# Optimization experiments

Measured on AMD Instinct MI355X. Metric: run time of the kernel, lower is better.

The kernel has to match this reference:

```python
import jax, jax.numpy as jnp
import numpy as np

N_NODES = 50000   # total nodes across batched graphs
N_EDGES = 100000  # molecular-like sparsity, avg degree ~2
N_GRAPHS = 2048
NUM_FEAT = 14
DIM = 64

def _gru_cell(x, h, w_ih, w_hh, b_ih, b_hh):
    # torch GRU gate order: reset, update, new
    gi = x @ w_ih.T + b_ih
    gh = h @ w_hh.T + b_hh
    ir, iz, in_ = jnp.split(gi, 3, axis=-1)
    hr, hz, hn = jnp.split(gh, 3, axis=-1)
    r = jax.nn.sigmoid(ir + hr)
    z = jax.nn.sigmoid(iz + hz)
    n = jnp.tanh(in_ + r * hn)
    return (1.0 - z) * n + z * h

def _lstm_cell(x, h, c, w_ih, w_hh, b_ih, b_hh):
    # torch LSTM gate order: input, forget, cell, output
    g = x @ w_ih.T + b_ih + h @ w_hh.T + b_hh
    i, f, gg, o = jnp.split(g, 4, axis=-1)
    c2 = jax.nn.sigmoid(f) * c + jax.nn.sigmoid(i) * jnp.tanh(gg)
    h2 = jax.nn.sigmoid(o) * jnp.tanh(c2)
    return h2, c2

def _forward(x, edge_attr, lin0_w, lin0_b, nn_w1, nn_b1, nn_w2, nn_b2,
             conv_root, conv_bias, gru_w_ih, gru_w_hh, gru_b_ih, gru_b_hh,
             s2s_w_ih, s2s_w_hh, s2s_b_ih, s2s_b_hh, lin1_w, lin1_b,
             lin2_w, lin2_b, edge_index, batch):
    N, D = x.shape[0], DIM
    src, dst = edge_index[0], edge_index[1]
    out = jax.nn.relu(x @ lin0_w.T + lin0_b)  # [N, D]
    h = out
    # edge-conditioned weight matrices: [E, D, D]
    ew = (jax.nn.relu(edge_attr @ nn_w1.T + nn_b1) @ nn_w2.T + nn_b2).reshape(-1, D, D)
    deg = jax.ops.segment_sum(jnp.ones_like(src, jnp.float32), dst, num_segments=N)
    inv_deg = 1.0 / jnp.maximum(deg, 1.0)
    for _ in range(3):
        msg = jnp.einsum('ei,eio->eo', out[src], ew)  # per-edge matvec
        agg = jax.ops.segment_sum(msg, dst, num_segments=N) * inv_deg[:, None]
        m = jax.nn.relu(out @ conv_root + agg + conv_bias)
        h = _gru_cell(m, h, gru_w_ih, gru_w_hh, gru_b_ih, gru_b_hh)
        out = h
    # Set2Set pooling, processing_steps=3
    B = N_GRAPHS
    q_star = jnp.zeros((B, 2 * D), x.dtype)
    hh = jnp.zeros((B, D), x.dtype)
    cc = jnp.zeros((B, D), x.dtype)
    for _ in range(3):
        hh, cc = _lstm_cell(q_star, hh, cc, s2s_w_ih, s2s_w_hh, s2s_b_ih, s2s_b_hh)
        e = jnp.sum(out * hh[batch], axis=-1)  # [N]
        e = e - jax.ops.segment_max(e, batch, num_segments=B)[batch]
        a = jnp.exp(e)
        a = a / (jax.ops.segment_sum(a, batch, num_segments=B)[batch] + 1e-16)
        r = jax.ops.segment_sum(a[:, None] * out, batch, num_segments=B)
        q_star = jnp.concatenate([hh, r], axis=-1)  # [B, 2D]
    y = jax.nn.relu(q_star @ lin1_w.T + lin1_b)
    y = y @ lin2_w.T + lin2_b
    return y.reshape(-1)

def setup_inputs():
    key = jax.random.key(0)
    ks = jax.random.split(key, 16)
    def rn(k, shape, scale=0.1):
        return jax.random.normal(k, shape, jnp.float32) * scale
    D = DIM
    return {
        'x': jax.random.normal(ks[0], (N_NODES, NUM_FEAT), jnp.float32),
        'edge_index': jax.random.randint(ks[1], (2, N_EDGES), 0, N_NODES),
        'edge_attr': jax.random.normal(ks[2], (N_EDGES, 4), jnp.float32),
        'batch': jnp.sort(jax.random.randint(ks[3], (N_NODES,), 0, N_GRAPHS)),
        'lin0_w': rn(ks[4], (D, NUM_FEAT)), 'lin0_b': jnp.zeros((D,), jnp.float32),
        'nn_w1': rn(ks[5], (128, 4)), 'nn_b1': jnp.zeros((128,), jnp.float32),
        'nn_w2': rn(ks[6], (D * D, 128), 0.02), 'nn_b2': jnp.zeros((D * D,), jnp.float32),
        'conv_root': rn(ks[7], (D, D)), 'conv_bias': jnp.zeros((D,), jnp.float32),
        'gru_w_ih': rn(ks[8], (3 * D, D)), 'gru_w_hh': rn(ks[9], (3 * D, D)),
        'gru_b_ih': jnp.zeros((3 * D,), jnp.float32), 'gru_b_hh': jnp.zeros((3 * D,), jnp.float32),
        's2s_w_ih': rn(ks[10], (4 * D, 2 * D)), 's2s_w_hh': rn(ks[11], (4 * D, D)),
        's2s_b_ih': jnp.zeros((4 * D,), jnp.float32), 's2s_b_hh': jnp.zeros((4 * D,), jnp.float32),
        'lin1_w': rn(ks[12], (D, 2 * D)), 'lin1_b': jnp.zeros((D,), jnp.float32),
        'lin2_w': rn(ks[13], (1, D)), 'lin2_b': jnp.zeros((1,), jnp.float32),
    }

def reference(x, edge_index, edge_attr, batch, lin0_w, lin0_b, nn_w1, nn_b1,
              nn_w2, nn_b2, conv_root, conv_bias, gru_w_ih, gru_w_hh, gru_b_ih,
              gru_b_hh, s2s_w_ih, s2s_w_hh, s2s_b_ih, s2s_b_hh, lin1_w, lin1_b,
              lin2_w, lin2_b):
    return _forward(x, edge_attr, lin0_w, lin0_b, nn_w1, nn_b1, nn_w2, nn_b2,
                    conv_root, conv_bias, gru_w_ih, gru_w_hh, gru_b_ih, gru_b_hh,
                    s2s_w_ih, s2s_w_hh, s2s_b_ih, s2s_b_hh, lin1_w, lin1_b,
                    lin2_w, lin2_b, edge_index, batch)
```

## Files before the change

### kernel.cpp

```cpp
#include <hip/hip_runtime.h>
#include <hip/hip_bf16.h>

#define NN 50000
#define NE 100000
#define NG 2048
#define NF 14
#define D 64
#define EB 128

typedef __attribute__((ext_vector_type(8))) short bf16x8;
typedef __attribute__((ext_vector_type(4))) float f32x4;

__device__ __forceinline__ float sigmoidf(float x) { return 1.f / (1.f + expf(-x)); }

__global__ void cvt_bf16_kernel(const float* __restrict__ src, __hip_bfloat16* __restrict__ dst, int n) {
    int i = blockIdx.x * 256 + threadIdx.x;
    if (i < n) dst[i] = __float2bfloat16(src[i]);
}

__global__ void transpose_kernel(const float* __restrict__ src, float* __restrict__ dst,
                                 int rows, int cols) {
    int idx = blockIdx.x * 256 + threadIdx.x;
    if (idx < rows * cols) {
        int r = idx / cols, c = idx - r * cols;
        dst[c * rows + r] = src[idx];
    }
}

__global__ void lin0_kernel(const float* __restrict__ x, const float* __restrict__ w,
                            const float* __restrict__ b, float* __restrict__ out) {
    int grp = threadIdx.x >> 6;
    int d = threadIdx.x & 63;
    int n = blockIdx.x * 4 + grp;
    __shared__ float xs[4][NF];
    int t = threadIdx.x;
    if (t < 4 * NF) {
        int r = t / NF, c = t - r * NF;
        int nn2 = blockIdx.x * 4 + r;
        xs[r][c] = (nn2 < NN) ? x[nn2 * NF + c] : 0.f;
    }
    __syncthreads();
    if (n >= NN) return;
    float acc = b[d];
#pragma unroll
    for (int k = 0; k < NF; k++) acc += xs[grp][k] * w[d * NF + k];
    out[n * D + d] = fmaxf(acc, 0.f);
}

__global__ __launch_bounds__(512, 4) void msg_mfma_kernel(
    const float* __restrict__ h, const float* __restrict__ ea,
    const float* __restrict__ w1, const float* __restrict__ b1,
    const __hip_bfloat16* __restrict__ w2r,
    const float* __restrict__ b2, const int* __restrict__ ei,
    float* __restrict__ agg)
{
    __shared__ __align__(16) char upool[34816];
    __hip_bfloat16 (*hid)[136] = (__hip_bfloat16(*)[136])upool;
    __hip_bfloat16 (*Bs)[64][136] = (__hip_bfloat16(*)[64][136])upool;
    __hip_bfloat16 (*B2s)[72] = (__hip_bfloat16(*)[72])upool;
    __shared__ __align__(16) float hsrcT[64][132];
    __shared__ float w1s[128][4];
    __shared__ float b1s[128];
    __shared__ int didx[EB];

    int tid = threadIdx.x;
    int e0 = blockIdx.x * EB;

    if (tid < 128) {
        didx[tid] = (e0 + tid < NE) ? ei[NE + e0 + tid] : -1;
    } else if (tid < 256) {
        int k = tid - 128;
        w1s[k][0] = w1[k * 4 + 0]; w1s[k][1] = w1[k * 4 + 1];
        w1s[k][2] = w1[k * 4 + 2]; w1s[k][3] = w1[k * 4 + 3];
        b1s[k] = b1[k];
    }
    {
        int e = tid >> 2, seg = (tid & 3) * 16;
        int ge = e0 + e;
        int src = (ge < NE) ? ei[ge] : 0;
        const float4* hp = (const float4*)(h + (size_t)src * 64 + seg);
#pragma unroll
        for (int u = 0; u < 4; u++) {
            float4 v = (ge < NE) ? hp[u] : make_float4(0.f, 0.f, 0.f, 0.f);
            hsrcT[seg + u * 4 + 0][e] = v.x;
            hsrcT[seg + u * 4 + 1][e] = v.y;
            hsrcT[seg + u * 4 + 2][e] = v.z;
            hsrcT[seg + u * 4 + 3][e] = v.w;
        }
    }
    __syncthreads();
    {
        int e = tid & 127, kb = (tid >> 7) * 32;
        int ge = e0 + e;
        float4 av = (ge < NE) ? *(const float4*)(ea + (size_t)ge * 4)
                              : make_float4(0.f, 0.f, 0.f, 0.f);
        for (int k = kb; k < kb + 32; k += 4) {
            union { __hip_bfloat16 b[4]; uint2 uu; } pk;
#pragma unroll
            for (int u = 0; u < 4; u++) {
                float v = b1s[k + u] + av.x * w1s[k + u][0] + av.y * w1s[k + u][1] +
                          av.z * w1s[k + u][2] + av.w * w1s[k + u][3];
                pk.b[u] = __float2bfloat16(fmaxf(v, 0.f));
            }
            *(uint2*)&hid[e][k] = pk.uu;
        }
    }
    __syncthreads();

    int lane = tid & 63;
    int wid = tid >> 6;
    int half = wid >> 2;
    int ct = wid & 3;
    int n = lane & 15, q = lane >> 4;
    int ocol = ct * 16 + n;

    bf16x8 afr[4][4];
#pragma unroll
    for (int rt = 0; rt < 4; rt++)
#pragma unroll
        for (int ks = 0; ks < 4; ks++)
            afr[rt][ks] = *(const bf16x8*)&hid[half * 64 + rt * 16 + n][ks * 32 + q * 8];
    __syncthreads();

    int srow = tid >> 3, sseg = (tid & 7) * 16;
    {
        const bf16x8* gp = (const bf16x8*)(w2r + (size_t)srow * 128 + sseg);
        bf16x8* lp = (bf16x8*)&Bs[0][srow][sseg];
        lp[0] = gp[0]; lp[1] = gp[1];
    }
    __syncthreads();

    f32x4 acc[4];
#pragma unroll
    for (int rt = 0; rt < 4; rt++) acc[rt] = (f32x4){0.f, 0.f, 0.f, 0.f};

    for (int i = 0; i < 64; i++) {
        const int cur = i & 1;
        bf16x8 pre0, pre1;
        if (i + 1 < 64) {
            const bf16x8* gp = (const bf16x8*)(w2r + (size_t)(i + 1) * 8192 + srow * 128 + sseg);
            pre0 = gp[0]; pre1 = gp[1];
        }
        bf16x8 bfr[4];
#pragma unroll
        for (int ks = 0; ks < 4; ks++)
            bfr[ks] = *(const bf16x8*)&Bs[cur][ocol][ks * 32 + q * 8];
        f32x4 S[4];
#pragma unroll
        for (int rt = 0; rt < 4; rt++) S[rt] = (f32x4){0.f, 0.f, 0.f, 0.f};
#pragma unroll
        for (int ks = 0; ks < 4; ks++)
#pragma unroll
            for (int rt = 0; rt < 4; rt++)
                S[rt] = __builtin_amdgcn_mfma_f32_16x16x32_bf16(afr[rt][ks], bfr[ks], S[rt], 0, 0, 0);
#pragma unroll
        for (int rt = 0; rt < 4; rt++) {
            f32x4 hm = *(const f32x4*)&hsrcT[i][half * 64 + rt * 16 + q * 4];
#pragma unroll
            for (int r = 0; r < 4; r++) acc[rt][r] += hm[r] * S[rt][r];
        }
        if (i + 1 < 64) {
            bf16x8* lp = (bf16x8*)&Bs[cur ^ 1][srow][sseg];
            lp[0] = pre0; lp[1] = pre1;
        }
        __syncthreads();
    }

    for (int g = tid; g < 4096; g += 512) {
        B2s[g & 63][g >> 6] = __float2bfloat16(b2[g]);
    }
    __syncthreads();
#pragma unroll
    for (int rt = 0; rt < 4; rt++) {
        f32x4 S2 = (f32x4){0.f, 0.f, 0.f, 0.f};
#pragma unroll
        for (int ks2 = 0; ks2 < 2; ks2++) {
            union { __hip_bfloat16 b[8]; bf16x8 v; } pk;
#pragma unroll
            for (int j = 0; j < 8; j++)
                pk.b[j] = __float2bfloat16(hsrcT[ks2 * 32 + q * 8 + j][half * 64 + rt * 16 + n]);
            bf16x8 bfr2 = *(const bf16x8*)&B2s[ocol][ks2 * 32 + q * 8];
            S2 = __builtin_amdgcn_mfma_f32_16x16x32_bf16(pk.v, bfr2, S2, 0, 0, 0);
        }
#pragma unroll
        for (int r = 0; r < 4; r++) acc[rt][r] += S2[r];
    }

#pragma unroll
    for (int rt = 0; rt < 4; rt++)
#pragma unroll
        for (int r = 0; r < 4; r++) {
            int e = half * 64 + rt * 16 + q * 4 + r;
            if (e0 + e < NE) {
                int dn = didx[e];
                atomicAdd(&agg[(size_t)dn * 64 + ocol], acc[rt][r]);
            }
        }
}

__global__ void deg_kernel(const int* __restrict__ ei, float* __restrict__ deg) {
    int e = blockIdx.x * 256 + threadIdx.x;
    if (e < NE) atomicAdd(&deg[ei[NE + e]], 1.0f);
}
__global__ void invdeg_kernel(float* deg) {
    int n = blockIdx.x * 256 + threadIdx.x;
    if (n < NN) deg[n] = 1.0f / fmaxf(deg[n], 1.0f);
}

__global__ __launch_bounds__(256) void conv_gru_kernel(
    float* __restrict__ h, const float* __restrict__ agg, const float* __restrict__ invdeg,
    const float* __restrict__ root, const float* __restrict__ cbias,
    const float* __restrict__ wihT, const float* __restrict__ whhT,
    const float* __restrict__ bih, const float* __restrict__ bhh)
{
    int tid = threadIdx.x;
    int grp = tid >> 6;
    int j = tid & 63;
    int n0 = blockIdx.x * 16;
    int nd0 = grp * 4;
    __shared__ float hs[16][64];
    __shared__ float ms[16][68];
    for (int i = tid; i < 1024; i += 256) {
        int nd = i >> 6, dd = i & 63;
        hs[nd][dd] = h[(n0 + nd) * D + dd];
    }
    __syncthreads();
    float mm[4] = {};
#pragma unroll 8
    for (int k = 0; k < 64; k++) {
        float rv = root[k * 64 + j];
#pragma unroll
        for (int q = 0; q < 4; q++) mm[q] += hs[nd0 + q][k] * rv;
    }
    float cb = cbias[j];
#pragma unroll
    for (int q = 0; q < 4; q++) {
        int nn2 = n0 + nd0 + q;
        float v = mm[q] + agg[(size_t)nn2 * 64 + j] * invdeg[nn2] + cb;
        ms[nd0 + q][j] = fmaxf(v, 0.f);
    }
    __syncthreads();
    float air[4] = {}, aiz[4] = {}, ain[4] = {};
    float ahr[4] = {}, ahz[4] = {}, ahn[4] = {};
#pragma unroll 4
    for (int k = 0; k < 64; k++) {
        float wr = wihT[k * 192 + j];
        float wz = wihT[k * 192 + 64 + j];
        float wn = wihT[k * 192 + 128 + j];
        float vr = whhT[k * 192 + j];
        float vz = whhT[k * 192 + 64 + j];
        float vn = whhT[k * 192 + 128 + j];
#pragma unroll
        for (int q = 0; q < 4; q++) {
            float mv = ms[nd0 + q][k], hv = hs[nd0 + q][k];
            air[q] = fmaf(mv, wr, air[q]);
            aiz[q] = fmaf(mv, wz, aiz[q]);
            ain[q] = fmaf(mv, wn, ain[q]);
            ahr[q] = fmaf(hv, vr, ahr[q]);
            ahz[q] = fmaf(hv, vz, ahz[q]);
            ahn[q] = fmaf(hv, vn, ahn[q]);
        }
    }
    float br = bih[j], bz = bih[64 + j], bn = bih[128 + j];
    float cr = bhh[j], cz = bhh[64 + j], cn = bhh[128 + j];
#pragma unroll
    for (int q = 0; q < 4; q++) {
        float r = sigmoidf(air[q] + br + ahr[q] + cr);
        float z = sigmoidf(aiz[q] + bz + ahz[q] + cz);
        float nn2 = tanhf(ain[q] + bn + r * (ahn[q] + cn));
        float hv = hs[nd0 + q][j];
        h[(n0 + nd0 + q) * D + j] = (1.f - z) * nn2 + z * hv;
    }
}

__global__ void starts_kernel(const int* __restrict__ batch, int* __restrict__ start) {
    int n = blockIdx.x * 256 + threadIdx.x;
    if (n >= NN) return;
    int b = batch[n];
    int bp = (n == 0) ? -1 : batch[n - 1];
    for (int g = bp + 1; g <= b; g++) start[g] = n;
    if (n == NN - 1) {
        for (int g = b + 1; g <= NG; g++) start[g] = NN;
    }
}

__global__ void s2s_lstm_kernel(const float* __restrict__ qstar, float* __restrict__ hh,
                                float* __restrict__ cc, const float* __restrict__ wihT,
                                const float* __restrict__ whhT, const float* __restrict__ bih,
                                const float* __restrict__ bhh) {
    int g = blockIdx.x;
    int j = threadIdx.x;
    __shared__ float q[128], hsh[64], gates[256];
    if (j < 128) q[j] = qstar[g * 128 + j];
    if (j < 64) hsh[j] = hh[g * 64 + j];
    __syncthreads();
    float acc = bih[j] + bhh[j];
#pragma unroll 8
    for (int k = 0; k < 128; k++) acc = fmaf(q[k], wihT[k * 256 + j], acc);
#pragma unroll 8
    for (int k = 0; k < 64; k++) acc = fmaf(hsh[k], whhT[k * 256 + j], acc);
    gates[j] = acc;
    __syncthreads();
    if (j < 64) {
        float gi = gates[j], gf = gates[64 + j], gg = gates[128 + j], go = gates[192 + j];
        float c2 = sigmoidf(gf) * cc[g * 64 + j] + sigmoidf(gi) * tanhf(gg);
        float h2 = sigmoidf(go) * tanhf(c2);
        cc[g * 64 + j] = c2;
        hh[g * 64 + j] = h2;
    }
}

__global__ void s2s_attn_kernel(const float* __restrict__ out, const float* __restrict__ hh,
                                const int* __restrict__ start, float* __restrict__ qstar) {
    int g = blockIdx.x;
    int tid = threadIdx.x;
    int d = tid & 63, sub = tid >> 6;
    int n0 = start[g], n1 = start[g + 1];
    float hd = hh[g * 64 + d];
    __shared__ float red[4][64];
    __shared__ float mxS[4], seS[4];
    float mx = -INFINITY;
    for (int n = n0 + sub; n < n1; n += 4) {
        float p = out[n * D + d] * hd;
#pragma unroll
        for (int off = 32; off; off >>= 1) p += __shfl_xor(p, off);
        mx = fmaxf(mx, p);
    }
    if (d == 0) mxS[sub] = mx;
    __syncthreads();
    mx = fmaxf(fmaxf(mxS[0], mxS[1]), fmaxf(mxS[2], mxS[3]));
    float sexp = 0.f, racc = 0.f;
    for (int n = n0 + sub; n < n1; n += 4) {
        float ond = out[n * D + d];
        float p = ond * hd;
#pragma unroll
        for (int off = 32; off; off >>= 1) p += __shfl_xor(p, off);
        float a = expf(p - mx);
        sexp += a;
        racc = fmaf(a, ond, racc);
    }
    red[sub][d] = racc;
    if (d == 0) seS[sub] = sexp;
    __syncthreads();
    if (sub == 0) {
        float rtot = red[0][d] + red[1][d] + red[2][d] + red[3][d];
        float stot = seS[0] + seS[1] + seS[2] + seS[3];
        float r = rtot / (stot + 1e-16f);
        qstar[g * 128 + d] = hd;
        qstar[g * 128 + 64 + d] = r;
    }
}

__global__ void final_kernel(const float* __restrict__ qstar, const float* __restrict__ w1,
                             const float* __restrict__ b1, const float* __restrict__ w2,
                             const float* __restrict__ b2, float* __restrict__ y) {
    int g = blockIdx.x;
    int d = threadIdx.x;
    __shared__ float q[128];
    q[d] = qstar[g * 128 + d];
    q[64 + d] = qstar[g * 128 + 64 + d];
    __syncthreads();
    float acc = b1[d];
#pragma unroll 8
    for (int k = 0; k < 128; k++) acc = fmaf(q[k], w1[d * 128 + k], acc);
    acc = fmaxf(acc, 0.f);
    float p = acc * w2[d];
#pragma unroll
    for (int off = 32; off; off >>= 1) p += __shfl_xor(p, off);
    if (d == 0) y[g] = p + b2[0];
}

extern "C" void kernel_launch(void* const* d_in, const int* in_sizes, int n_in,
                              void* d_out, int out_size, void* d_ws, size_t ws_size,
                              hipStream_t stream) {
    (void)in_sizes; (void)n_in; (void)out_size; (void)ws_size;
    const float* x = (const float*)d_in[0];
    const int* edge_index = (const int*)d_in[1];
    const float* edge_attr = (const float*)d_in[2];
    const int* batch = (const int*)d_in[3];
    const float* lin0_w = (const float*)d_in[4];
    const float* lin0_b = (const float*)d_in[5];
    const float* nn_w1 = (const float*)d_in[6];
    const float* nn_b1 = (const float*)d_in[7];
    const float* nn_w2 = (const float*)d_in[8];
    const float* nn_b2 = (const float*)d_in[9];
    const float* conv_root = (const float*)d_in[10];
    const float* conv_bias = (const float*)d_in[11];
    const float* gru_w_ih = (const float*)d_in[12];
    const float* gru_w_hh = (const float*)d_in[13];
    const float* gru_b_ih = (const float*)d_in[14];
    const float* gru_b_hh = (const float*)d_in[15];
    const float* s2s_w_ih = (const float*)d_in[16];
    const float* s2s_w_hh = (const float*)d_in[17];
    const float* s2s_b_ih = (const float*)d_in[18];
    const float* s2s_b_hh = (const float*)d_in[19];
    const float* lin1_w = (const float*)d_in[20];
    const float* lin1_b = (const float*)d_in[21];
    const float* lin2_w = (const float*)d_in[22];
    const float* lin2_b = (const float*)d_in[23];
    float* y = (float*)d_out;

    char* ws = (char*)d_ws;
    size_t off = 0;
    auto alloc = [&](size_t bytes) {
        void* p = ws + off;
        off = (off + bytes + 255) & ~(size_t)255;
        return p;
    };
    float* h = (float*)alloc((size_t)NN * D * 4);
    float* agg = (float*)alloc((size_t)NN * D * 4);
    float* invdeg = (float*)alloc((size_t)NN * 4);
    int* start = (int*)alloc((size_t)(NG + 1) * 4);
    float* qstar = (float*)alloc((size_t)NG * 128 * 4);
    float* hh = (float*)alloc((size_t)NG * 64 * 4);
    float* ccv = (float*)alloc((size_t)NG * 64 * 4);
    float* gruT_ih = (float*)alloc(192 * 64 * 4);
    float* gruT_hh = (float*)alloc(192 * 64 * 4);
    float* s2sT_ih = (float*)alloc(256 * 128 * 4);
    float* s2sT_hh = (float*)alloc(256 * 64 * 4);
    __hip_bfloat16* w2r = (__hip_bfloat16*)qstar;

    hipMemsetAsync(invdeg, 0, (size_t)NN * 4, stream);
    transpose_kernel<<<(192 * 64 + 255) / 256, 256, 0, stream>>>(gru_w_ih, gruT_ih, 192, 64);
    transpose_kernel<<<(192 * 64 + 255) / 256, 256, 0, stream>>>(gru_w_hh, gruT_hh, 192, 64);
    transpose_kernel<<<(256 * 128 + 255) / 256, 256, 0, stream>>>(s2s_w_ih, s2sT_ih, 256, 128);
    transpose_kernel<<<(256 * 64 + 255) / 256, 256, 0, stream>>>(s2s_w_hh, s2sT_hh, 256, 64);
    cvt_bf16_kernel<<<(64 * 8192 + 255) / 256, 256, 0, stream>>>(nn_w2, w2r, 64 * 8192);
    lin0_kernel<<<NN / 4, 256, 0, stream>>>(x, lin0_w, lin0_b, h);
    deg_kernel<<<(NE + 255) / 256, 256, 0, stream>>>(edge_index, invdeg);
    invdeg_kernel<<<(NN + 255) / 256, 256, 0, stream>>>(invdeg);
    starts_kernel<<<(NN + 255) / 256, 256, 0, stream>>>(batch, start);

    for (int it = 0; it < 3; it++) {
        hipMemsetAsync(agg, 0, (size_t)NN * D * 4, stream);
        msg_mfma_kernel<<<(NE + EB - 1) / EB, 512, 0, stream>>>(
            h, edge_attr, nn_w1, nn_b1, w2r, nn_b2, edge_index, agg);
        conv_gru_kernel<<<NN / 16, 256, 0, stream>>>(
            h, agg, invdeg, conv_root, conv_bias, gruT_ih, gruT_hh, gru_b_ih, gru_b_hh);
    }

    hipMemsetAsync(qstar, 0, (size_t)NG * 128 * 4, stream);
    hipMemsetAsync(hh, 0, (size_t)NG * 64 * 4, stream);
    hipMemsetAsync(ccv, 0, (size_t)NG * 64 * 4, stream);
    for (int t = 0; t < 3; t++) {
        s2s_lstm_kernel<<<NG, 256, 0, stream>>>(qstar, hh, ccv, s2sT_ih, s2sT_hh, s2s_b_ih, s2s_b_hh);
        s2s_attn_kernel<<<NG, 256, 0, stream>>>(h, hh, start, qstar);
    }
    final_kernel<<<NG, 64, 0, stream>>>(qstar, lin1_w, lin1_b, lin2_w, lin2_b, y);
}
```

Measured before the change: 811.7 us.

## Stream swizzled bf16 edge-net weights into LDS with async global_load_lds

A new setup kernel converts the second edge-network weight to bf16 in an XOR-style swizzled layout. The message kernel then streams each weight slice straight into LDS with async global-to-LDS copies instead of staging it through registers, and reads B fragments without padding-based bank-conflict avoidance. The edge tile drops to 64 edges on 256 threads, and gathered source features are held as bf16 in LDS, which shrinks shared memory and register use and allows more resident blocks. In exchange, each block now re-streams the whole weight tensor for half as many edges, and source features lose precision in the per-edge products.

```diff
diff --git a/kernel.cpp b/kernel.cpp
--- a/kernel.cpp
+++ b/kernel.cpp
@@ -6,16 +6,28 @@
 #define NG 2048
 #define NF 14
 #define D 64
-#define EB 128
+#define EB 64
 
 typedef __attribute__((ext_vector_type(8))) short bf16x8;
 typedef __attribute__((ext_vector_type(4))) float f32x4;
+typedef unsigned int u32;
 
 __device__ __forceinline__ float sigmoidf(float x) { return 1.f / (1.f + expf(-x)); }
 
-__global__ void cvt_bf16_kernel(const float* __restrict__ src, __hip_bfloat16* __restrict__ dst, int n) {
-    int i = blockIdx.x * 256 + threadIdx.x;
-    if (i < n) dst[i] = __float2bfloat16(src[i]);
+__device__ __forceinline__ void async_copy16(void* lds, const void* g) {
+    __builtin_amdgcn_global_load_lds(
+        (const __attribute__((address_space(1))) u32*)g,
+        (__attribute__((address_space(3))) u32*)lds, 16, 0, 0);
+}
+
+__global__ void swz_w2_kernel(const float* __restrict__ w2, __hip_bfloat16* __restrict__ w2s) {
+    int t = blockIdx.x * 256 + threadIdx.x;
+    int i = t >> 10, o = (t >> 4) & 63, c = t & 15;
+    const float* src = w2 + ((size_t)(i * 64 + o)) * 128 + c * 8;
+    union { __hip_bfloat16 b[8]; uint4 u; } pk;
+#pragma unroll
+    for (int j = 0; j < 8; j++) pk.b[j] = __float2bfloat16(src[j]);
+    *(uint4*)((char*)w2s + (size_t)i * 16384 + o * 256 + ((c + o) & 15) * 16) = pk.u;
 }
 
 __global__ void transpose_kernel(const float* __restrict__ src, float* __restrict__ dst,
@@ -47,18 +59,17 @@
     out[n * D + d] = fmaxf(acc, 0.f);
 }
 
-__global__ __launch_bounds__(512, 4) void msg_mfma_kernel(
+__global__ __launch_bounds__(256, 3) void msg_mfma_kernel(
     const float* __restrict__ h, const float* __restrict__ ea,
     const float* __restrict__ w1, const float* __restrict__ b1,
-    const __hip_bfloat16* __restrict__ w2r,
+    const __hip_bfloat16* __restrict__ w2s,
     const float* __restrict__ b2, const int* __restrict__ ei,
     float* __restrict__ agg)
 {
-    __shared__ __align__(16) char upool[34816];
-    __hip_bfloat16 (*hid)[136] = (__hip_bfloat16(*)[136])upool;
-    __hip_bfloat16 (*Bs)[64][136] = (__hip_bfloat16(*)[64][136])upool;
-    __hip_bfloat16 (*B2s)[72] = (__hip_bfloat16(*)[72])upool;
-    __shared__ __align__(16) float hsrcT[64][132];
+    __shared__ __align__(16) char pool[32768];
+    __hip_bfloat16 (*hid)[136] = (__hip_bfloat16(*)[136])pool;
+    __hip_bfloat16 (*B2s)[72] = (__hip_bfloat16(*)[72])pool;
+    __shared__ __align__(16) __hip_bfloat16 hsT[64][72];
     __shared__ float w1s[128][4];
     __shared__ float b1s[128];
     __shared__ int didx[EB];
@@ -66,31 +77,31 @@
     int tid = threadIdx.x;
     int e0 = blockIdx.x * EB;
 
-    if (tid < 128) {
+    if (tid < EB) {
         didx[tid] = (e0 + tid < NE) ? ei[NE + e0 + tid] : -1;
-    } else if (tid < 256) {
-        int k = tid - 128;
+    } else if (tid < EB + 128) {
+        int k = tid - EB;
         w1s[k][0] = w1[k * 4 + 0]; w1s[k][1] = w1[k * 4 + 1];
         w1s[k][2] = w1[k * 4 + 2]; w1s[k][3] = w1[k * 4 + 3];
         b1s[k] = b1[k];
     }
     {
-        int e = tid >> 2, seg = (tid & 3) * 16;
+        int e = tid >> 2, sg = (tid & 3) * 16;
         int ge = e0 + e;
         int src = (ge < NE) ? ei[ge] : 0;
-        const float4* hp = (const float4*)(h + (size_t)src * 64 + seg);
+        const float4* hp = (const float4*)(h + (size_t)src * 64 + sg);
 #pragma unroll
         for (int u = 0; u < 4; u++) {
             float4 v = (ge < NE) ? hp[u] : make_float4(0.f, 0.f, 0.f, 0.f);
-            hsrcT[seg + u * 4 + 0][e] = v.x;
-            hsrcT[seg + u * 4 + 1][e] = v.y;
-            hsrcT[seg + u * 4 + 2][e] = v.z;
-            hsrcT[seg + u * 4 + 3][e] = v.w;
+            hsT[sg + u * 4 + 0][e] = __float2bfloat16(v.x);
+            hsT[sg + u * 4 + 1][e] = __float2bfloat16(v.y);
+            hsT[sg + u * 4 + 2][e] = __float2bfloat16(v.z);
+            hsT[sg + u * 4 + 3][e] = __float2bfloat16(v.w);
         }
     }
     __syncthreads();
     {
-        int e = tid & 127, kb = (tid >> 7) * 32;
+        int e = tid & 63, kb = (tid >> 6) * 32;
         int ge = e0 + e;
         float4 av = (ge < NE) ? *(const float4*)(ea + (size_t)ge * 4)
                               : make_float4(0.f, 0.f, 0.f, 0.f);
@@ -100,7 +111,7 @@
             for (int u = 0; u < 4; u++) {
                 float v = b1s[k + u] + av.x * w1s[k + u][0] + av.y * w1s[k + u][1] +
                           av.z * w1s[k + u][2] + av.w * w1s[k + u][3];
-                pk.b[u] = __float2bfloat16(fmaxf(v, 0.f));
+                pk.b[u] = __float2bfloat16((ge < NE) ? fmaxf(v, 0.f) : 0.f);
             }
             *(uint2*)&hid[e][k] = pk.uu;
         }
@@ -109,24 +120,27 @@
 
     int lane = tid & 63;
     int wid = tid >> 6;
-    int half = wid >> 2;
-    int ct = wid & 3;
     int n = lane & 15, q = lane >> 4;
-    int ocol = ct * 16 + n;
+    int ocol = wid * 16 + n;
 
     bf16x8 afr[4][4];
 #pragma unroll
     for (int rt = 0; rt < 4; rt++)
 #pragma unroll
         for (int ks = 0; ks < 4; ks++)
-            afr[rt][ks] = *(const bf16x8*)&hid[half * 64 + rt * 16 + n][ks * 32 + q * 8];
-    __syncthreads();
-
-    int srow = tid >> 3, sseg = (tid & 7) * 16;
+            afr[rt][ks] = *(const bf16x8*)&hid[rt * 16 + n][ks * 32 + q * 8];
+    __syncthreads();
+
+    int boff[4];
+#pragma unroll
+    for (int ks = 0; ks < 4; ks++)
+        boff[ks] = ocol * 256 + (((ks * 4 + q) + ocol) & 15) * 16;
+
     {
-        const bf16x8* gp = (const bf16x8*)(w2r + (size_t)srow * 128 + sseg);
-        bf16x8* lp = (bf16x8*)&Bs[0][srow][sseg];
-        lp[0] = gp[0]; lp[1] = gp[1];
+        const char* g = (const char*)w2s + (size_t)wid * 4096 + lane * 16;
+        char* l = pool + wid * 4096;
+#pragma unroll
+        for (int j = 0; j < 4; j++) async_copy16(l + j * 1024, g + j * 1024);
     }
     __syncthreads();
 
@@ -136,38 +150,40 @@
 
     for (int i = 0; i < 64; i++) {
         const int cur = i & 1;
-        bf16x8 pre0, pre1;
+        char* bbase = pool + cur * 16384;
         if (i + 1 < 64) {
-            const bf16x8* gp = (const bf16x8*)(w2r + (size_t)(i + 1) * 8192 + srow * 128 + sseg);
-            pre0 = gp[0]; pre1 = gp[1];
-        }
-        bf16x8 bfr[4];
-#pragma unroll
-        for (int ks = 0; ks < 4; ks++)
-            bfr[ks] = *(const bf16x8*)&Bs[cur][ocol][ks * 32 + q * 8];
+            const char* g = (const char*)w2s + (size_t)(i + 1) * 16384 + wid * 4096 + lane * 16;
+            char* l = pool + (cur ^ 1) * 16384 + wid * 4096;
+#pragma unroll
+            for (int j = 0; j < 4; j++) async_copy16(l + j * 1024, g + j * 1024);
+        }
         f32x4 S[4];
 #pragma unroll
         for (int rt = 0; rt < 4; rt++) S[rt] = (f32x4){0.f, 0.f, 0.f, 0.f};
 #pragma unroll
-        for (int ks = 0; ks < 4; ks++)
+        for (int ks = 0; ks < 4; ks++) {
+            bf16x8 bfr = *(const bf16x8*)(bbase + boff[ks]);
 #pragma unroll
             for (int rt = 0; rt < 4; rt++)
-                S[rt] = __builtin_amdgcn_mfma_f32_16x16x32_bf16(afr[rt][ks], bfr[ks], S[rt], 0, 0, 0);
+                S[rt] = __builtin_amdgcn_mfma_f32_16x16x32_bf16(afr[rt][ks], bfr, S[rt], 0, 0, 0);
+        }
 #pragma unroll
         for (int rt = 0; rt < 4; rt++) {
-            f32x4 hm = *(const f32x4*)&hsrcT[i][half * 64 + rt * 16 + q * 4];
-#pragma unroll
-            for (int r = 0; r < 4; r++) acc[rt][r] += hm[r] * S[rt][r];
-        }
-        if (i + 1 < 64) {
-            bf16x8* lp = (bf16x8*)&Bs[cur ^ 1][srow][sseg];
-            lp[0] = pre0; lp[1] = pre1;
+            uint2 hm = *(const uint2*)&hsT[i][rt * 16 + q * 4];
+            float m0 = __uint_as_float(hm.x << 16);
+            float m1 = __uint_as_float(hm.x & 0xffff0000u);
+            float m2 = __uint_as_float(hm.y << 16);
+            float m3 = __uint_as_float(hm.y & 0xffff0000u);
+            acc[rt][0] += m0 * S[rt][0];
+            acc[rt][1] += m1 * S[rt][1];
+            acc[rt][2] += m2 * S[rt][2];
+            acc[rt][3] += m3 * S[rt][3];
         }
         __syncthreads();
     }
 
-    for (int g = tid; g < 4096; g += 512) {
-        B2s[g & 63][g >> 6] = __float2bfloat16(b2[g]);
+    for (int g2 = tid; g2 < 4096; g2 += 256) {
+        B2s[g2 & 63][g2 >> 6] = __float2bfloat16(b2[g2]);
     }
     __syncthreads();
 #pragma unroll
@@ -178,7 +194,7 @@
             union { __hip_bfloat16 b[8]; bf16x8 v; } pk;
 #pragma unroll
             for (int j = 0; j < 8; j++)
-                pk.b[j] = __float2bfloat16(hsrcT[ks2 * 32 + q * 8 + j][half * 64 + rt * 16 + n]);
+                pk.b[j] = hsT[ks2 * 32 + q * 8 + j][rt * 16 + n];
             bf16x8 bfr2 = *(const bf16x8*)&B2s[ocol][ks2 * 32 + q * 8];
             S2 = __builtin_amdgcn_mfma_f32_16x16x32_bf16(pk.v, bfr2, S2, 0, 0, 0);
         }
@@ -190,11 +206,9 @@
     for (int rt = 0; rt < 4; rt++)
 #pragma unroll
         for (int r = 0; r < 4; r++) {
-            int e = half * 64 + rt * 16 + q * 4 + r;
-            if (e0 + e < NE) {
-                int dn = didx[e];
-                atomicAdd(&agg[(size_t)dn * 64 + ocol], acc[rt][r]);
-            }
+            int e = rt * 16 + q * 4 + r;
+            int dn = didx[e];
+            if (dn >= 0) atomicAdd(&agg[(size_t)dn * 64 + ocol], acc[rt][r]);
         }
 }
 
@@ -418,14 +432,14 @@
     float* gruT_hh = (float*)alloc(192 * 64 * 4);
     float* s2sT_ih = (float*)alloc(256 * 128 * 4);
     float* s2sT_hh = (float*)alloc(256 * 64 * 4);
-    __hip_bfloat16* w2r = (__hip_bfloat16*)qstar;
+    __hip_bfloat16* w2s = (__hip_bfloat16*)qstar;
 
     hipMemsetAsync(invdeg, 0, (size_t)NN * 4, stream);
     transpose_kernel<<<(192 * 64 + 255) / 256, 256, 0, stream>>>(gru_w_ih, gruT_ih, 192, 64);
     transpose_kernel<<<(192 * 64 + 255) / 256, 256, 0, stream>>>(gru_w_hh, gruT_hh, 192, 64);
     transpose_kernel<<<(256 * 128 + 255) / 256, 256, 0, stream>>>(s2s_w_ih, s2sT_ih, 256, 128);
     transpose_kernel<<<(256 * 64 + 255) / 256, 256, 0, stream>>>(s2s_w_hh, s2sT_hh, 256, 64);
-    cvt_bf16_kernel<<<(64 * 8192 + 255) / 256, 256, 0, stream>>>(nn_w2, w2r, 64 * 8192);
+    swz_w2_kernel<<<256, 256, 0, stream>>>(nn_w2, w2s);
     lin0_kernel<<<NN / 4, 256, 0, stream>>>(x, lin0_w, lin0_b, h);
     deg_kernel<<<(NE + 255) / 256, 256, 0, stream>>>(edge_index, invdeg);
     invdeg_kernel<<<(NN + 255) / 256, 256, 0, stream>>>(invdeg);
@@ -433,8 +447,8 @@
 
     for (int it = 0; it < 3; it++) {
         hipMemsetAsync(agg, 0, (size_t)NN * D * 4, stream);
-        msg_mfma_kernel<<<(NE + EB - 1) / EB, 512, 0, stream>>>(
-            h, edge_attr, nn_w1, nn_b1, w2r, nn_b2, edge_index, agg);
+        msg_mfma_kernel<<<(NE + EB - 1) / EB, 256, 0, stream>>>(
+            h, edge_attr, nn_w1, nn_b1, w2s, nn_b2, edge_index, agg);
         conv_gru_kernel<<<NN / 16, 256, 0, stream>>>(
             h, agg, invdeg, conv_root, conv_bias, gruT_ih, gruT_hh, gru_b_ih, gru_b_hh);
     }
```

Result: slower. 921.0 us (+13.5%).

## Double edges per block and read W2 fragments directly from global memory

Applied to the files above, without the earlier changes.

The message kernel now handles 256 edges per block, so each wave holds 8 row tiles and each streamed W2 slice is reused across twice as many edges. The shared-memory double buffer for W2 and its per-iteration __syncthreads are removed; each lane prefetches its B fragments straight from global (L2-resident) memory into registers. The conv-GRU kernel also moves to 32 nodes per 512-thread block with bounds checks. The cost is more registers (afr[8][4], acc[8]) and about 67KB of LDS, which lowers occupancy to 2 blocks per CU. There are also redundant global reads of W2 across waves instead of shared staging.

```diff
diff --git a/kernel.cpp b/kernel.cpp
--- a/kernel.cpp
+++ b/kernel.cpp
@@ -6,7 +6,7 @@
 #define NG 2048
 #define NF 14
 #define D 64
-#define EB 128
+#define EB 256
 
 typedef __attribute__((ext_vector_type(8))) short bf16x8;
 typedef __attribute__((ext_vector_type(4))) float f32x4;
@@ -47,18 +47,17 @@
     out[n * D + d] = fmaxf(acc, 0.f);
 }
 
-__global__ __launch_bounds__(512, 4) void msg_mfma_kernel(
+__global__ __launch_bounds__(512, 2) void msg_mfma_kernel(
     const float* __restrict__ h, const float* __restrict__ ea,
     const float* __restrict__ w1, const float* __restrict__ b1,
     const __hip_bfloat16* __restrict__ w2r,
     const float* __restrict__ b2, const int* __restrict__ ei,
     float* __restrict__ agg)
 {
-    __shared__ __align__(16) char upool[34816];
-    __hip_bfloat16 (*hid)[136] = (__hip_bfloat16(*)[136])upool;
-    __hip_bfloat16 (*Bs)[64][136] = (__hip_bfloat16(*)[64][136])upool;
-    __hip_bfloat16 (*B2s)[72] = (__hip_bfloat16(*)[72])upool;
-    __shared__ __align__(16) float hsrcT[64][132];
+    __shared__ __align__(16) char pool[67584];
+    __hip_bfloat16 (*hid)[132] = (__hip_bfloat16(*)[132])pool;
+    __hip_bfloat16 (*B2s)[72] = (__hip_bfloat16(*)[72])pool;
+    __shared__ __align__(16) float hsT[64][260];
     __shared__ float w1s[128][4];
     __shared__ float b1s[128];
     __shared__ int didx[EB];
@@ -67,40 +66,38 @@
     int e0 = blockIdx.x * EB;
 
     if (tid < 128) {
-        didx[tid] = (e0 + tid < NE) ? ei[NE + e0 + tid] : -1;
-    } else if (tid < 256) {
-        int k = tid - 128;
-        w1s[k][0] = w1[k * 4 + 0]; w1s[k][1] = w1[k * 4 + 1];
-        w1s[k][2] = w1[k * 4 + 2]; w1s[k][3] = w1[k * 4 + 3];
-        b1s[k] = b1[k];
-    }
+        w1s[tid][0] = w1[tid * 4 + 0]; w1s[tid][1] = w1[tid * 4 + 1];
+        w1s[tid][2] = w1[tid * 4 + 2]; w1s[tid][3] = w1[tid * 4 + 3];
+        b1s[tid] = b1[tid];
+    }
+    if (tid < EB) didx[tid] = (e0 + tid < NE) ? ei[NE + e0 + tid] : -1;
     {
-        int e = tid >> 2, seg = (tid & 3) * 16;
+        int e = tid >> 1, half = (tid & 1) * 32;
         int ge = e0 + e;
         int src = (ge < NE) ? ei[ge] : 0;
-        const float4* hp = (const float4*)(h + (size_t)src * 64 + seg);
-#pragma unroll
-        for (int u = 0; u < 4; u++) {
+        const float4* hp = (const float4*)(h + (size_t)src * 64 + half);
+#pragma unroll
+        for (int u = 0; u < 8; u++) {
             float4 v = (ge < NE) ? hp[u] : make_float4(0.f, 0.f, 0.f, 0.f);
-            hsrcT[seg + u * 4 + 0][e] = v.x;
-            hsrcT[seg + u * 4 + 1][e] = v.y;
-            hsrcT[seg + u * 4 + 2][e] = v.z;
-            hsrcT[seg + u * 4 + 3][e] = v.w;
+            hsT[half + u * 4 + 0][e] = v.x;
+            hsT[half + u * 4 + 1][e] = v.y;
+            hsT[half + u * 4 + 2][e] = v.z;
+            hsT[half + u * 4 + 3][e] = v.w;
         }
     }
     __syncthreads();
     {
-        int e = tid & 127, kb = (tid >> 7) * 32;
+        int e = tid & 255, kb = (tid >> 8) * 64;
         int ge = e0 + e;
         float4 av = (ge < NE) ? *(const float4*)(ea + (size_t)ge * 4)
                               : make_float4(0.f, 0.f, 0.f, 0.f);
-        for (int k = kb; k < kb + 32; k += 4) {
+        for (int k = kb; k < kb + 64; k += 4) {
             union { __hip_bfloat16 b[4]; uint2 uu; } pk;
 #pragma unroll
             for (int u = 0; u < 4; u++) {
                 float v = b1s[k + u] + av.x * w1s[k + u][0] + av.y * w1s[k + u][1] +
                           av.z * w1s[k + u][2] + av.w * w1s[k + u][3];
-                pk.b[u] = __float2bfloat16(fmaxf(v, 0.f));
+                pk.b[u] = __float2bfloat16((ge < NE) ? fmaxf(v, 0.f) : 0.f);
             }
             *(uint2*)&hid[e][k] = pk.uu;
         }
@@ -114,71 +111,61 @@
     int n = lane & 15, q = lane >> 4;
     int ocol = ct * 16 + n;
 
-    bf16x8 afr[4][4];
-#pragma unroll
-    for (int rt = 0; rt < 4; rt++)
+    bf16x8 afr[8][4];
+#pragma unroll
+    for (int rt = 0; rt < 8; rt++)
 #pragma unroll
         for (int ks = 0; ks < 4; ks++)
-            afr[rt][ks] = *(const bf16x8*)&hid[half * 64 + rt * 16 + n][ks * 32 + q * 8];
-    __syncthreads();
-
-    int srow = tid >> 3, sseg = (tid & 7) * 16;
-    {
-        const bf16x8* gp = (const bf16x8*)(w2r + (size_t)srow * 128 + sseg);
-        bf16x8* lp = (bf16x8*)&Bs[0][srow][sseg];
-        lp[0] = gp[0]; lp[1] = gp[1];
-    }
-    __syncthreads();
-
-    f32x4 acc[4];
-#pragma unroll
-    for (int rt = 0; rt < 4; rt++) acc[rt] = (f32x4){0.f, 0.f, 0.f, 0.f};
+            afr[rt][ks] = *(const bf16x8*)&hid[half * 128 + rt * 16 + n][ks * 32 + q * 8];
+
+    const __hip_bfloat16* bptr = w2r + (size_t)ocol * 128 + q * 8;
+
+    f32x4 acc[8];
+#pragma unroll
+    for (int rt = 0; rt < 8; rt++) acc[rt] = (f32x4){0.f, 0.f, 0.f, 0.f};
+
+    bf16x8 bcur[4], bnxt[4];
+#pragma unroll
+    for (int ks = 0; ks < 4; ks++) bcur[ks] = *(const bf16x8*)(bptr + ks * 32);
 
     for (int i = 0; i < 64; i++) {
-        const int cur = i & 1;
-        bf16x8 pre0, pre1;
         if (i + 1 < 64) {
-            const bf16x8* gp = (const bf16x8*)(w2r + (size_t)(i + 1) * 8192 + srow * 128 + sseg);
-            pre0 = gp[0]; pre1 = gp[1];
-        }
-        bf16x8 bfr[4];
+            const __hip_bfloat16* p = bptr + (size_t)(i + 1) * 8192;
+#pragma unroll
+            for (int ks = 0; ks < 4; ks++) bnxt[ks] = *(const bf16x8*)(p + ks * 32);
+        }
+        f32x4 S[8];
+#pragma unroll
+        for (int rt = 0; rt < 8; rt++) S[rt] = (f32x4){0.f, 0.f, 0.f, 0.f};
 #pragma unroll
         for (int ks = 0; ks < 4; ks++)
-            bfr[ks] = *(const bf16x8*)&Bs[cur][ocol][ks * 32 + q * 8];
-        f32x4 S[4];
-#pragma unroll
-        for (int rt = 0; rt < 4; rt++) S[rt] = (f32x4){0.f, 0.f, 0.f, 0.f};
-#pragma unroll
-        for (int ks = 0; ks < 4; ks++)
-#pragma unroll
-            for (int rt = 0; rt < 4; rt++)
-                S[rt] = __builtin_amdgcn_mfma_f32_16x16x32_bf16(afr[rt][ks], bfr[ks], S[rt], 0, 0, 0);
-#pragma unroll
-        for (int rt = 0; rt < 4; rt++) {
-            f32x4 hm = *(const f32x4*)&hsrcT[i][half * 64 + rt * 16 + q * 4];
+#pragma unroll
+            for (int rt = 0; rt < 8; rt++)
+                S[rt] = __builtin_amdgcn_mfma_f32_16x16x32_bf16(afr[rt][ks], bcur[ks], S[rt], 0, 0, 0);
+#pragma unroll
+        for (int rt = 0; rt < 8; rt++) {
+            f32x4 hm = *(const f32x4*)&hsT[i][half * 128 + rt * 16 + q * 4];
 #pragma unroll
             for (int r = 0; r < 4; r++) acc[rt][r] += hm[r] * S[rt][r];
         }
-        if (i + 1 < 64) {
-            bf16x8* lp = (bf16x8*)&Bs[cur ^ 1][srow][sseg];
-            lp[0] = pre0; lp[1] = pre1;
-        }
-        __syncthreads();
-    }
-
-    for (int g = tid; g < 4096; g += 512) {
-        B2s[g & 63][g >> 6] = __float2bfloat16(b2[g]);
-    }
-    __syncthreads();
-#pragma unroll
-    for (int rt = 0; rt < 4; rt++) {
+#pragma unroll
+        for (int ks = 0; ks < 4; ks++) bcur[ks] = bnxt[ks];
+    }
+
+    __syncthreads();
+    for (int g2 = tid; g2 < 4096; g2 += 512) {
+        B2s[g2 & 63][g2 >> 6] = __float2bfloat16(b2[g2]);
+    }
+    __syncthreads();
+#pragma unroll
+    for (int rt = 0; rt < 8; rt++) {
         f32x4 S2 = (f32x4){0.f, 0.f, 0.f, 0.f};
 #pragma unroll
         for (int ks2 = 0; ks2 < 2; ks2++) {
             union { __hip_bfloat16 b[8]; bf16x8 v; } pk;
 #pragma unroll
             for (int j = 0; j < 8; j++)
-                pk.b[j] = __float2bfloat16(hsrcT[ks2 * 32 + q * 8 + j][half * 64 + rt * 16 + n]);
+                pk.b[j] = __float2bfloat16(hsT[ks2 * 32 + q * 8 + j][half * 128 + rt * 16 + n]);
             bf16x8 bfr2 = *(const bf16x8*)&B2s[ocol][ks2 * 32 + q * 8];
             S2 = __builtin_amdgcn_mfma_f32_16x16x32_bf16(pk.v, bfr2, S2, 0, 0, 0);
         }
@@ -187,14 +174,12 @@
     }
 
 #pragma unroll
-    for (int rt = 0; rt < 4; rt++)
+    for (int rt = 0; rt < 8; rt++)
 #pragma unroll
         for (int r = 0; r < 4; r++) {
-            int e = half * 64 + rt * 16 + q * 4 + r;
-            if (e0 + e < NE) {
-                int dn = didx[e];
-                atomicAdd(&agg[(size_t)dn * 64 + ocol], acc[rt][r]);
-            }
+            int e = half * 128 + rt * 16 + q * 4 + r;
+            int dn = didx[e];
+            if (dn >= 0) atomicAdd(&agg[(size_t)dn * 64 + ocol], acc[rt][r]);
         }
 }
 
@@ -207,7 +192,7 @@
     if (n < NN) deg[n] = 1.0f / fmaxf(deg[n], 1.0f);
 }
 
-__global__ __launch_bounds__(256) void conv_gru_kernel(
+__global__ __launch_bounds__(512) void conv_gru_kernel(
     float* __restrict__ h, const float* __restrict__ agg, const float* __restrict__ invdeg,
     const float* __restrict__ root, const float* __restrict__ cbias,
     const float* __restrict__ wihT, const float* __restrict__ whhT,
@@ -216,13 +201,14 @@
     int tid = threadIdx.x;
     int grp = tid >> 6;
     int j = tid & 63;
-    int n0 = blockIdx.x * 16;
+    int n0 = blockIdx.x * 32;
     int nd0 = grp * 4;
-    __shared__ float hs[16][64];
-    __shared__ float ms[16][68];
-    for (int i = tid; i < 1024; i += 256) {
+    __shared__ float hs[32][64];
+    __shared__ float ms[32][68];
+    for (int i = tid; i < 2048; i += 512) {
         int nd = i >> 6, dd = i & 63;
-        hs[nd][dd] = h[(n0 + nd) * D + dd];
+        int nn2 = n0 + nd;
+        hs[nd][dd] = (nn2 < NN) ? h[(size_t)nn2 * D + dd] : 0.f;
     }
     __syncthreads();
     float mm[4] = {};
@@ -236,8 +222,9 @@
 #pragma unroll
     for (int q = 0; q < 4; q++) {
         int nn2 = n0 + nd0 + q;
-        float v = mm[q] + agg[(size_t)nn2 * 64 + j] * invdeg[nn2] + cb;
-        ms[nd0 + q][j] = fmaxf(v, 0.f);
+        float v = 0.f;
+        if (nn2 < NN) v = fmaxf(mm[q] + agg[(size_t)nn2 * 64 + j] * invdeg[nn2] + cb, 0.f);
+        ms[nd0 + q][j] = v;
     }
     __syncthreads();
     float air[4] = {}, aiz[4] = {}, ain[4] = {};
@@ -265,11 +252,13 @@
     float cr = bhh[j], cz = bhh[64 + j], cn = bhh[128 + j];
 #pragma unroll
     for (int q = 0; q < 4; q++) {
+        int nn2 = n0 + nd0 + q;
+        if (nn2 >= NN) continue;
         float r = sigmoidf(air[q] + br + ahr[q] + cr);
         float z = sigmoidf(aiz[q] + bz + ahz[q] + cz);
-        float nn2 = tanhf(ain[q] + bn + r * (ahn[q] + cn));
+        float nv = tanhf(ain[q] + bn + r * (ahn[q] + cn));
         float hv = hs[nd0 + q][j];
-        h[(n0 + nd0 + q) * D + j] = (1.f - z) * nn2 + z * hv;
+        h[(size_t)nn2 * D + j] = (1.f - z) * nv + z * hv;
     }
 }
 
@@ -435,7 +424,7 @@
         hipMemsetAsync(agg, 0, (size_t)NN * D * 4, stream);
         msg_mfma_kernel<<<(NE + EB - 1) / EB, 512, 0, stream>>>(
             h, edge_attr, nn_w1, nn_b1, w2r, nn_b2, edge_index, agg);
-        conv_gru_kernel<<<NN / 16, 256, 0, stream>>>(
+        conv_gru_kernel<<<(NN + 31) / 32, 512, 0, stream>>>(
             h, agg, invdeg, conv_root, conv_bias, gruT_ih, gruT_hh, gru_b_ih, gru_b_hh);
     }
 
```

Measured after the change: 981.7 us. 21.0% more time.
